# Performance work log

Hardware: AMD Instinct MI355X
Metric: run time of the kernel (lower is better)

Reference implementation:

```python
import jax, jax.numpy as jnp
import numpy as np

DICE_TH = 0.4
CLS_TH = 0.5
LN_EPS = 1e-5


def setup_inputs() -> dict:
    key = jax.random.key(0)
    P, C, NC, K = 200_000, 256, 200, 24  # points, clicks, classes, latent prototypes
    ks = jax.random.split(key, 6)
    # structured masks: each click targets one of K prototype regions so the
    # dice/cls thresholds yield a non-degenerate grouping
    point_proto = jax.random.randint(ks[0], (P,), 0, K)
    proto_vals = jax.random.uniform(ks[1], (P,))
    click_proto = jax.random.randint(ks[2], (C,), 0, K)
    base = (point_proto[:, None] == click_proto[None, :]).astype(jnp.float32)  # [P, C]
    noise = jax.random.uniform(ks[3], (P, C))
    masks_heatmap = base * (0.6 + 0.4 * proto_vals[:, None]) + 0.02 * noise
    class_emb = jax.random.normal(ks[4], (K, NC)) * 3.0
    cls_logits = class_emb[click_proto] + 0.3 * jax.random.normal(ks[5], (C, NC))
    clicks_list = jax.random.randint(ks[0], (C,), 0, NC)  # unused (random_clicks=True)
    return {"masks_heatmap": masks_heatmap, "cls_logits": cls_logits,
            "clicks_list": clicks_list}


def _associate(masks_heatmap, cls_logits):
    """Greedy dice+cls-similarity grouping (random_clicks=True path).
    Returns labels[c] = leader click index of the group containing click c."""
    M = masks_heatmap                      # [P, C]
    C = M.shape[1]
    s = M.sum(0)                           # [C]
    # dice[i, j] = 2 * m_i . m_j / (sum(m_i) + sum(m_j))  (all pairs at once)
    dice = 2.0 * (M.T @ M) / (s[:, None] + s[None, :])
    # F.layer_norm over last dim, no affine
    mu = cls_logits.mean(-1, keepdims=True)
    var = ((cls_logits - mu) ** 2).mean(-1, keepdims=True)
    p = (cls_logits - mu) / jnp.sqrt(var + LN_EPS)
    sim = p @ p.T                          # [C, C]
    cond = (dice > DICE_TH) & (sim > CLS_TH)

    def step(carry, x):
        assigned, labels = carry
        i, row = x
        # skip if i already suppressed; take unsuppressed clicks matching row i
        take = row & (~assigned) & (~assigned[i])
        return (assigned | take, jnp.where(take, i, labels)), None

    init = (jnp.zeros((C,), bool), jnp.full((C,), -1, jnp.int32))
    (assigned, labels), _ = jax.lax.scan(
        step, init, (jnp.arange(C, dtype=jnp.int32), cond))
    return labels


def _merge(labels, masks_heatmap, cls_logits):
    """reduction='max': per-group max over member clicks. Unused group slots
    (non-leader indices) are zero-filled and flagged by group_valid."""
    C = masks_heatmap.shape[1]
    seg = jnp.where(labels >= 0, labels, C)  # route unassigned to dump segment
    counts = jax.ops.segment_sum(jnp.ones((C,), jnp.float32), seg,
                                 num_segments=C + 1)[:C]
    group_valid = counts > 0
    nm = jax.ops.segment_max(masks_heatmap.T, seg, num_segments=C + 1)[:C]  # [C, P]
    nc = jax.ops.segment_max(cls_logits, seg, num_segments=C + 1)[:C]      # [C, NC]
    new_masks = jnp.where(group_valid[:, None], nm, 0.0).T  # [P, C]
    new_cls = jnp.where(group_valid[:, None], nc, 0.0)      # [C, NC]
    return new_masks, new_cls, group_valid


def reference(masks_heatmap, cls_logits, clicks_list):
    labels = _associate(masks_heatmap, cls_logits)
    new_masks, new_cls, group_valid = _merge(labels, masks_heatmap, cls_logits)
    return labels, group_valid, new_masks, new_cls
```

## Files before the change

kernel.cpp:

```cpp
#include <hip/hip_runtime.h>
#include <cstdint>
#include <cstddef>

constexpr int P  = 200000;
constexpr int C  = 256;
constexpr int NC = 200;
#define DICE_TH 0.4f
#define CLS_TH  0.5f
#define LN_EPS  1e-5f

constexpr int KC = 1600;
constexpr int NCHUNK = 125;
constexpr int NSTEP = KC / 32;

constexpr size_t WS_G       = 0;
constexpr size_t WS_S       = 262144;
constexpr size_t WS_PROW    = 263168;
constexpr size_t WS_PT      = 467968;
constexpr size_t WS_COND    = 672768;
constexpr size_t WS_MSTART  = 680960;
constexpr size_t WS_MEMBERS = 682240;
constexpr size_t WS_PART    = 1048576;
constexpr size_t PART_BYTES = (size_t)NCHUNK * 3 * 16384 * 4;

typedef float floatx4 __attribute__((ext_vector_type(4)));
typedef float floatx16 __attribute__((ext_vector_type(16)));
typedef __bf16 bf16x4 __attribute__((ext_vector_type(4)));
typedef __bf16 bf16x8 __attribute__((ext_vector_type(8)));
typedef unsigned short ushort4v __attribute__((ext_vector_type(4)));
typedef unsigned short ushort8 __attribute__((ext_vector_type(8)));

constexpr int LDA = 40;

__global__ __launch_bounds__(256, 2) void gram_mfma_kernel(
    const float* __restrict__ M, float* __restrict__ G, float* __restrict__ s,
    float* __restrict__ part) {
  __shared__ unsigned short Abf[128 * LDA];
  __shared__ unsigned short Bbf[128 * LDA];
  __shared__ float scol[128];

  const int type = blockIdx.x;
  const int i0 = (type == 2) ? 128 : 0;
  const int j0 = (type == 0) ? 0 : 128;
  const bool diag = (type != 1);
  const int tid = threadIdx.x;
  const int wv = tid >> 6, lane = tid & 63;
  const int wr = wv >> 1, wc = wv & 1;
  const int g  = tid & 31;
  const int kq = tid >> 5;
  const int chunk = blockIdx.y;
  const int k0 = chunk * KC;

  if (tid < 128) scol[tid] = 0.f;

  floatx16 acc[4];
#pragma unroll
  for (int t = 0; t < 4; ++t)
#pragma unroll
    for (int r = 0; r < 16; ++r) acc[t][r] = 0.f;
  float ss[4] = {0.f, 0.f, 0.f, 0.f};

  const int mrow = lane & 31;
  const int kgrp = (lane >> 5) * 8;
  const int xa = ((mrow >> 2) & 3) << 1;
  const int wbase = (kq ^ ((g & 3) << 1)) << 2;

  const float* baseA = M + i0 + 4 * g;
  const float* baseB = M + j0 + 4 * g;

#define LOADS(dst, base, step_)                                              \
  {                                                                          \
    const float* src_ = (base) + (size_t)(k0 + (step_) * 32 + 4 * kq) * 256; \
    dst[0] = *reinterpret_cast<const floatx4*>(src_);                        \
    dst[1] = *reinterpret_cast<const floatx4*>(src_ + 256);                  \
    dst[2] = *reinterpret_cast<const floatx4*>(src_ + 512);                  \
    dst[3] = *reinterpret_cast<const floatx4*>(src_ + 768);                  \
  }

#define STAGE(dstLds, r_)                                                    \
  {                                                                          \
    _Pragma("unroll") for (int cc = 0; cc < 4; ++cc) {                       \
      floatx4 f = {r_[0][cc], r_[1][cc], r_[2][cc], r_[3][cc]};              \
      bf16x4 b = __builtin_convertvector(f, bf16x4);                         \
      *reinterpret_cast<ushort4v*>(&dstLds[(4 * g + cc) * LDA + wbase]) =    \
          __builtin_bit_cast(ushort4v, b);                                   \
    }                                                                        \
  }

#define SSUM(r_)                                                             \
  if (diag) {                                                                \
    ss[0] += r_[0][0] + r_[1][0] + r_[2][0] + r_[3][0];                      \
    ss[1] += r_[0][1] + r_[1][1] + r_[2][1] + r_[3][1];                      \
    ss[2] += r_[0][2] + r_[1][2] + r_[2][2] + r_[3][2];                      \
    ss[3] += r_[0][3] + r_[1][3] + r_[2][3] + r_[3][3];                      \
  }

#define MFMA_STEP()                                                          \
  {                                                                          \
    const unsigned short* Bsrc = diag ? Abf : Bbf;                           \
    _Pragma("unroll") for (int sub = 0; sub < 2; ++sub) {                    \
      const int ko = sub * 16 + kgrp;                                        \
      const int koff = (((ko >> 2) ^ xa) << 2);                              \
      bf16x8 av0 = __builtin_bit_cast(                                       \
          bf16x8, *reinterpret_cast<const ushort8*>(                         \
                      &Abf[(64 * wr + mrow) * LDA + koff]));                 \
      bf16x8 av1 = __builtin_bit_cast(                                       \
          bf16x8, *reinterpret_cast<const ushort8*>(                         \
                      &Abf[(64 * wr + 32 + mrow) * LDA + koff]));            \
      bf16x8 bv0 = __builtin_bit_cast(                                       \
          bf16x8, *reinterpret_cast<const ushort8*>(                         \
                      &Bsrc[(64 * wc + mrow) * LDA + koff]));                \
      bf16x8 bv1 = __builtin_bit_cast(                                       \
          bf16x8, *reinterpret_cast<const ushort8*>(                         \
                      &Bsrc[(64 * wc + 32 + mrow) * LDA + koff]));           \
      acc[0] = __builtin_amdgcn_mfma_f32_32x32x16_bf16(av0, bv0, acc[0], 0, 0, 0); \
      acc[1] = __builtin_amdgcn_mfma_f32_32x32x16_bf16(av0, bv1, acc[1], 0, 0, 0); \
      acc[2] = __builtin_amdgcn_mfma_f32_32x32x16_bf16(av1, bv0, acc[2], 0, 0, 0); \
      acc[3] = __builtin_amdgcn_mfma_f32_32x32x16_bf16(av1, bv1, acc[3], 0, 0, 0); \
    }                                                                        \
  }

  floatx4 a0[4], a1[4], b0[4], b1[4];
  LOADS(a0, baseA, 0);
  if (!diag) LOADS(b0, baseB, 0);

  for (int sp = 0; sp < NSTEP; sp += 2) {
    SSUM(a0);
    STAGE(Abf, a0);
    if (!diag) STAGE(Bbf, b0);
    __syncthreads();
    LOADS(a1, baseA, sp + 1);
    if (!diag) LOADS(b1, baseB, sp + 1);
    MFMA_STEP();
    __syncthreads();

    SSUM(a1);
    STAGE(Abf, a1);
    if (!diag) STAGE(Bbf, b1);
    __syncthreads();
    if (sp + 2 < NSTEP) {
      LOADS(a0, baseA, sp + 2);
      if (!diag) LOADS(b0, baseB, sp + 2);
    }
    MFMA_STEP();
    __syncthreads();
  }
#undef LOADS
#undef STAGE
#undef SSUM
#undef MFMA_STEP

  if (part != nullptr) {
    float* Pp = part + ((size_t)chunk * 3 + type) * 16384;
#pragma unroll
    for (int ai = 0; ai < 2; ++ai)
#pragma unroll
      for (int bj = 0; bj < 2; ++bj)
#pragma unroll
        for (int r = 0; r < 16; ++r) {
          const int lr = 64 * wr + 32 * ai + (r & 3) + 8 * (r >> 2) + 4 * (lane >> 5);
          const int lc = 64 * wc + 32 * bj + (lane & 31);
          Pp[lr * 128 + lc] = acc[ai * 2 + bj][r];
        }
  } else {
#pragma unroll
    for (int ai = 0; ai < 2; ++ai)
#pragma unroll
      for (int bj = 0; bj < 2; ++bj)
#pragma unroll
        for (int r = 0; r < 16; ++r) {
          const int gr = i0 + 64 * wr + 32 * ai + (r & 3) + 8 * (r >> 2) + 4 * (lane >> 5);
          const int gc = j0 + 64 * wc + 32 * bj + (lane & 31);
          atomicAdd(&G[(size_t)gr * 256 + gc], acc[ai * 2 + bj][r]);
        }
  }
  if (diag) {
#pragma unroll
    for (int cc = 0; cc < 4; ++cc) atomicAdd(&scol[4 * g + cc], ss[cc]);
    __syncthreads();
    if (tid < 128) atomicAdd(&s[i0 + tid], scol[tid]);
  }
}

__global__ __launch_bounds__(128) void reduce_g_kernel(
    const float* __restrict__ part, float* __restrict__ G) {
  const int slot = blockIdx.x >> 7;
  const int lr = blockIdx.x & 127;
  const int lc = threadIdx.x;
  const float* src = part + (size_t)slot * 16384 + (size_t)lr * 128 + lc;
  float s0 = 0.f, s1 = 0.f, s2 = 0.f, s3 = 0.f, s4 = 0.f;
  int ch = 0;
  for (; ch + 5 <= NCHUNK; ch += 5) {
    s0 += src[(size_t)(ch + 0) * 49152];
    s1 += src[(size_t)(ch + 1) * 49152];
    s2 += src[(size_t)(ch + 2) * 49152];
    s3 += src[(size_t)(ch + 3) * 49152];
    s4 += src[(size_t)(ch + 4) * 49152];
  }
  for (; ch < NCHUNK; ++ch) s0 += src[(size_t)ch * 49152];
  const int i0 = (slot == 2) ? 128 : 0;
  const int j0 = (slot == 0) ? 0 : 128;
  G[(size_t)(i0 + lr) * 256 + (j0 + lc)] = ((s0 + s1) + (s2 + s3)) + s4;
}

__global__ __launch_bounds__(64) void ln_kernel(const float* __restrict__ cls,
                                                float* __restrict__ p_row,
                                                float* __restrict__ pT) {
  const int c = blockIdx.x;
  const int t = threadIdx.x;
  const float* x = cls + (size_t)c * NC;
  float v0 = x[t];
  float v1 = x[t + 64];
  float v2 = (t < 72) ? x[t + 128] : 0.f;

  float sum = v0 + v1 + v2;
#pragma unroll
  for (int o = 32; o > 0; o >>= 1) sum += __shfl_xor(sum, o);
  const float mu = sum / (float)NC;

  float d0 = v0 - mu, d1 = v1 - mu, d2 = (t < 72) ? (v2 - mu) : 0.f;
  float sq = d0 * d0 + d1 * d1 + d2 * d2;
#pragma unroll
  for (int o = 32; o > 0; o >>= 1) sq += __shfl_xor(sq, o);
  const float var = sq / (float)NC;
  const float inv = 1.0f / sqrtf(var + LN_EPS);

  float p0 = d0 * inv, p1 = d1 * inv, p2 = d2 * inv;
  p_row[(size_t)c * NC + t] = p0;
  p_row[(size_t)c * NC + t + 64] = p1;
  pT[(size_t)t * C + c] = p0;
  pT[(size_t)(t + 64) * C + c] = p1;
  if (t < 72) {
    p_row[(size_t)c * NC + t + 128] = p2;
    pT[(size_t)(t + 128) * C + c] = p2;
  }
}

__global__ __launch_bounds__(256) void cond_kernel(
    const float* __restrict__ G, const float* __restrict__ s,
    const float* __restrict__ p_row, const float* __restrict__ pT,
    unsigned long long* __restrict__ condW) {
  __shared__ float pi[NC];
  const int i = blockIdx.x;
  const int j = threadIdx.x;
  if (j < NC) pi[j] = p_row[(size_t)i * NC + j];
  __syncthreads();

  const float si = s[i];
  const float sj = s[j];
  const float g = (i >= 128 && j < 128) ? G[(size_t)j * C + i]
                                        : G[(size_t)i * C + j];
  const float dice = 2.f * g / (si + sj);

  float acc = 0.f;
#pragma unroll 8
  for (int k = 0; k < NC; ++k) acc = fmaf(pi[k], pT[(size_t)k * C + j], acc);

  const bool cnd = (dice > DICE_TH) && (acc > CLS_TH);
  unsigned long long m = __ballot(cnd);
  if ((j & 63) == 0) condW[i * 4 + (j >> 6)] = m;
}

__global__ __launch_bounds__(64) void scan_kernel(
    const unsigned long long* __restrict__ condW,
    float* __restrict__ out_labels, float* __restrict__ out_valid,
    int* __restrict__ mstart, int* __restrict__ members) {
  __shared__ unsigned long long cS[C * 4];
  __shared__ int cnt[C];
  __shared__ int ms[C + 1];
  const int t = threadIdx.x;

  for (int idx = t; idx < C * 4; idx += 64) cS[idx] = condW[idx];
  for (int idx = t; idx < C; idx += 64) cnt[idx] = 0;
  __syncthreads();

  unsigned long long asg[4] = {0ull, 0ull, 0ull, 0ull};
  int lab[4] = {-1, -1, -1, -1};

#pragma unroll
  for (int w = 0; w < 4; ++w) {
    for (int b = 0; b < 64; ++b) {
      const int i = w * 64 + b;
      if (!((asg[w] >> b) & 1ull)) {
#pragma unroll
        for (int w2 = 0; w2 < 4; ++w2) {
          unsigned long long tk = cS[i * 4 + w2] & ~asg[w2];
          asg[w2] |= tk;
          if ((tk >> t) & 1ull) lab[w2] = i;
        }
      }
    }
  }

#pragma unroll
  for (int w = 0; w < 4; ++w)
    if (lab[w] >= 0) atomicAdd(&cnt[lab[w]], 1);
  __syncthreads();

  if (t == 0) {
    ms[0] = 0;
    for (int c2 = 0; c2 < C; ++c2) ms[c2 + 1] = ms[c2] + cnt[c2];
  }
  __syncthreads();
  for (int idx = t; idx < C; idx += 64) cnt[idx] = ms[idx];
  __syncthreads();
#pragma unroll
  for (int w = 0; w < 4; ++w) {
    if (lab[w] >= 0) {
      int pos = atomicAdd(&cnt[lab[w]], 1);
      members[pos] = w * 64 + t;
    }
  }
#pragma unroll
  for (int w = 0; w < 4; ++w) {
    const int col = w * 64 + t;
    out_labels[col] = (float)lab[w];
    out_valid[col] = (ms[col + 1] > ms[col]) ? 1.0f : 0.0f;
  }
  for (int idx = t; idx < C + 1; idx += 64) mstart[idx] = ms[idx];
}

constexpr int MROWS = 8;

__global__ __launch_bounds__(256) void merge_masks_kernel(
    const float* __restrict__ M, const int* __restrict__ mstart,
    const int* __restrict__ members, float* __restrict__ out_masks) {
  __shared__ float rows[MROWS * 256];
  __shared__ int msS[C + 1];
  __shared__ int memS[C];
  const int tid = threadIdx.x;
  const size_t p0 = (size_t)blockIdx.x * MROWS;

  msS[tid] = mstart[tid];
  if (tid == 0) msS[C] = mstart[C];
  memS[tid] = members[tid];

  const float4* src = reinterpret_cast<const float4*>(M + p0 * 256);
#pragma unroll
  for (int it = 0; it < MROWS / 4; ++it)
    reinterpret_cast<float4*>(rows)[it * 256 + tid] = src[it * 256 + tid];
  __syncthreads();

  const int st = msS[tid], en = msS[tid + 1];
  float mx[MROWS];
  if (en > st) {
    const int m0 = memS[st];
#pragma unroll
    for (int r = 0; r < MROWS; ++r) mx[r] = rows[r * 256 + m0];
    for (int k = st + 1; k < en; ++k) {
      const int mm = memS[k];
#pragma unroll
      for (int r = 0; r < MROWS; ++r) mx[r] = fmaxf(mx[r], rows[r * 256 + mm]);
    }
  } else {
#pragma unroll
    for (int r = 0; r < MROWS; ++r) mx[r] = 0.f;
  }
  __syncthreads();
#pragma unroll
  for (int r = 0; r < MROWS; ++r) rows[r * 256 + tid] = mx[r];
  __syncthreads();

  const int r2 = tid >> 6;
  const int cg = (tid & 63) << 2;
#pragma unroll
  for (int pass = 0; pass < MROWS / 4; ++pass) {
    const int rr = pass * 4 + r2;
    floatx4 v = *reinterpret_cast<const floatx4*>(&rows[rr * 256 + cg]);
    __builtin_nontemporal_store(
        v, reinterpret_cast<floatx4*>(&out_masks[(p0 + rr) * 256 + cg]));
  }
}

__global__ __launch_bounds__(256) void merge_cls_kernel(
    const float* __restrict__ cls, const int* __restrict__ mstart,
    const int* __restrict__ members, float* __restrict__ out_cls) {
  __shared__ int se[2];
  const int c = blockIdx.x;
  const int t = threadIdx.x;
  if (t < 2) se[t] = mstart[c + t];
  __syncthreads();
  const int st = se[0], en = se[1];
  if (t < NC) {
    float mx = 0.f;
    if (en > st) {
      mx = cls[(size_t)members[st] * NC + t];
      for (int k = st + 1; k < en; ++k)
        mx = fmaxf(mx, cls[(size_t)members[k] * NC + t]);
    }
    out_cls[(size_t)c * NC + t] = mx;
  }
}

extern "C" void kernel_launch(void* const* d_in, const int* in_sizes, int n_in,
                              void* d_out, int out_size, void* d_ws,
                              size_t ws_size, hipStream_t stream) {
  const float* M = (const float*)d_in[0];
  const float* cls = (const float*)d_in[1];

  float* out = (float*)d_out;
  char* ws = (char*)d_ws;
  float* G = (float*)(ws + WS_G);
  float* s = (float*)(ws + WS_S);
  float* p_row = (float*)(ws + WS_PROW);
  float* pT = (float*)(ws + WS_PT);
  unsigned long long* condW = (unsigned long long*)(ws + WS_COND);
  int* mstart = (int*)(ws + WS_MSTART);
  int* members = (int*)(ws + WS_MEMBERS);

  float* out_labels = out;
  float* out_valid = out + 256;
  float* out_masks = out + 512;
  float* out_cls = out + 512 + (size_t)P * 256;

  const bool bigws = ws_size >= WS_PART + PART_BYTES;
  float* part = bigws ? (float*)(ws + WS_PART) : nullptr;

  if (bigws) {
    hipMemsetAsync(ws + WS_S, 0, 1024, stream);
  } else {
    hipMemsetAsync(ws, 0, WS_S + 1024, stream);
  }

  gram_mfma_kernel<<<dim3(3, NCHUNK), 256, 0, stream>>>(M, G, s, part);
  if (bigws) reduce_g_kernel<<<384, 128, 0, stream>>>(part, G);
  ln_kernel<<<C, 64, 0, stream>>>(cls, p_row, pT);
  cond_kernel<<<C, 256, 0, stream>>>(G, s, p_row, pT, condW);
  scan_kernel<<<1, 64, 0, stream>>>(condW, out_labels, out_valid, mstart,
                                    members);
  merge_masks_kernel<<<P / MROWS, 256, 0, stream>>>(M, mstart, members,
                                                    out_masks);
  merge_cls_kernel<<<C, 256, 0, stream>>>(cls, mstart, members, out_cls);
}
```

Before: 419.4 us.

## Remap gram blocks for XCD locality and fuse partial reduction into cond kernel

The gram kernel now uses a 1D grid of 384 blocks. Blocks are remapped so that all three tile types of a chunk, and contiguous chunks, land on the same XCD (bid & 7), which improves L2 sharing of the M rows. The separate reduce_g launch is removed, and cond_kernel now sums the 125 per-chunk partials itself for each (i,j) element. This saves one launch and one round trip for G, but the partial reduction now runs in 256 blocks, with strided loads per thread in place of a dedicated kernel.

```diff
diff --git a/kernel.cpp b/kernel.cpp
--- a/kernel.cpp
+++ b/kernel.cpp
@@ -35,11 +35,21 @@
 __global__ __launch_bounds__(256, 2) void gram_mfma_kernel(
     const float* __restrict__ M, float* __restrict__ G, float* __restrict__ s,
     float* __restrict__ part) {
+  const int bid = blockIdx.x;
+  const int xcd = bid & 7;
+  const int slot = bid >> 3;
+  constexpr int q = NCHUNK / 8, r = NCHUNK % 8;
+  const int nch = (xcd < r) ? q + 1 : q;
+  const int ci = slot / 3;
+  if (ci >= nch) return;
+  const int cbase = (xcd < r) ? xcd * (q + 1) : r * (q + 1) + (xcd - r) * q;
+  const int chunk = cbase + ci;
+  const int type = slot - 3 * ci;
+
   __shared__ unsigned short Abf[128 * LDA];
   __shared__ unsigned short Bbf[128 * LDA];
   __shared__ float scol[128];
 
-  const int type = blockIdx.x;
   const int i0 = (type == 2) ? 128 : 0;
   const int j0 = (type == 0) ? 0 : 128;
   const bool diag = (type != 1);
@@ -48,7 +58,6 @@
   const int wr = wv >> 1, wc = wv & 1;
   const int g  = tid & 31;
   const int kq = tid >> 5;
-  const int chunk = blockIdx.y;
   const int k0 = chunk * KC;
 
   if (tid < 128) scol[tid] = 0.f;
@@ -57,7 +66,7 @@
 #pragma unroll
   for (int t = 0; t < 4; ++t)
 #pragma unroll
-    for (int r = 0; r < 16; ++r) acc[t][r] = 0.f;
+    for (int r2 = 0; r2 < 16; ++r2) acc[t][r2] = 0.f;
   float ss[4] = {0.f, 0.f, 0.f, 0.f};
 
   const int mrow = lane & 31;
@@ -157,10 +166,10 @@
 #pragma unroll
       for (int bj = 0; bj < 2; ++bj)
 #pragma unroll
-        for (int r = 0; r < 16; ++r) {
-          const int lr = 64 * wr + 32 * ai + (r & 3) + 8 * (r >> 2) + 4 * (lane >> 5);
+        for (int r2 = 0; r2 < 16; ++r2) {
+          const int lr = 64 * wr + 32 * ai + (r2 & 3) + 8 * (r2 >> 2) + 4 * (lane >> 5);
           const int lc = 64 * wc + 32 * bj + (lane & 31);
-          Pp[lr * 128 + lc] = acc[ai * 2 + bj][r];
+          Pp[lr * 128 + lc] = acc[ai * 2 + bj][r2];
         }
   } else {
 #pragma unroll
@@ -168,10 +177,10 @@
 #pragma unroll
       for (int bj = 0; bj < 2; ++bj)
 #pragma unroll
-        for (int r = 0; r < 16; ++r) {
-          const int gr = i0 + 64 * wr + 32 * ai + (r & 3) + 8 * (r >> 2) + 4 * (lane >> 5);
+        for (int r2 = 0; r2 < 16; ++r2) {
+          const int gr = i0 + 64 * wr + 32 * ai + (r2 & 3) + 8 * (r2 >> 2) + 4 * (lane >> 5);
           const int gc = j0 + 64 * wc + 32 * bj + (lane & 31);
-          atomicAdd(&G[(size_t)gr * 256 + gc], acc[ai * 2 + bj][r]);
+          atomicAdd(&G[(size_t)gr * 256 + gc], acc[ai * 2 + bj][r2]);
         }
   }
   if (diag) {
@@ -180,27 +189,6 @@
     __syncthreads();
     if (tid < 128) atomicAdd(&s[i0 + tid], scol[tid]);
   }
-}
-
-__global__ __launch_bounds__(128) void reduce_g_kernel(
-    const float* __restrict__ part, float* __restrict__ G) {
-  const int slot = blockIdx.x >> 7;
-  const int lr = blockIdx.x & 127;
-  const int lc = threadIdx.x;
-  const float* src = part + (size_t)slot * 16384 + (size_t)lr * 128 + lc;
-  float s0 = 0.f, s1 = 0.f, s2 = 0.f, s3 = 0.f, s4 = 0.f;
-  int ch = 0;
-  for (; ch + 5 <= NCHUNK; ch += 5) {
-    s0 += src[(size_t)(ch + 0) * 49152];
-    s1 += src[(size_t)(ch + 1) * 49152];
-    s2 += src[(size_t)(ch + 2) * 49152];
-    s3 += src[(size_t)(ch + 3) * 49152];
-    s4 += src[(size_t)(ch + 4) * 49152];
-  }
-  for (; ch < NCHUNK; ++ch) s0 += src[(size_t)ch * 49152];
-  const int i0 = (slot == 2) ? 128 : 0;
-  const int j0 = (slot == 0) ? 0 : 128;
-  G[(size_t)(i0 + lr) * 256 + (j0 + lc)] = ((s0 + s1) + (s2 + s3)) + s4;
 }
 
 __global__ __launch_bounds__(64) void ln_kernel(const float* __restrict__ cls,
@@ -237,20 +225,43 @@
 }
 
 __global__ __launch_bounds__(256) void cond_kernel(
-    const float* __restrict__ G, const float* __restrict__ s,
-    const float* __restrict__ p_row, const float* __restrict__ pT,
-    unsigned long long* __restrict__ condW) {
+    const float* __restrict__ G, const float* __restrict__ part,
+    const float* __restrict__ s, const float* __restrict__ p_row,
+    const float* __restrict__ pT, unsigned long long* __restrict__ condW) {
   __shared__ float pi[NC];
   const int i = blockIdx.x;
   const int j = threadIdx.x;
   if (j < NC) pi[j] = p_row[(size_t)i * NC + j];
   __syncthreads();
 
+  float gsum;
+  if (part != nullptr) {
+    int type, lr, lc;
+    if (i < 128) {
+      if (j < 128) { type = 0; lr = i; lc = j; }
+      else         { type = 1; lr = i; lc = j - 128; }
+    } else {
+      if (j >= 128) { type = 2; lr = i - 128; lc = j - 128; }
+      else          { type = 1; lr = j; lc = i - 128; }
+    }
+    const float* src = part + (size_t)type * 16384 + (size_t)lr * 128 + lc;
+    float s0 = 0.f, s1 = 0.f, s2 = 0.f, s3 = 0.f, s4 = 0.f;
+#pragma unroll 1
+    for (int ch = 0; ch + 5 <= NCHUNK; ch += 5) {
+      s0 += src[(size_t)(ch + 0) * 49152];
+      s1 += src[(size_t)(ch + 1) * 49152];
+      s2 += src[(size_t)(ch + 2) * 49152];
+      s3 += src[(size_t)(ch + 3) * 49152];
+      s4 += src[(size_t)(ch + 4) * 49152];
+    }
+    gsum = ((s0 + s1) + (s2 + s3)) + s4;
+  } else {
+    gsum = (i >= 128 && j < 128) ? G[(size_t)j * C + i] : G[(size_t)i * C + j];
+  }
+
   const float si = s[i];
   const float sj = s[j];
-  const float g = (i >= 128 && j < 128) ? G[(size_t)j * C + i]
-                                        : G[(size_t)i * C + j];
-  const float dice = 2.f * g / (si + sj);
+  const float dice = 2.f * gsum / (si + sj);
 
   float acc = 0.f;
 #pragma unroll 8
@@ -422,10 +433,9 @@
     hipMemsetAsync(ws, 0, WS_S + 1024, stream);
   }
 
-  gram_mfma_kernel<<<dim3(3, NCHUNK), 256, 0, stream>>>(M, G, s, part);
-  if (bigws) reduce_g_kernel<<<384, 128, 0, stream>>>(part, G);
+  gram_mfma_kernel<<<384, 256, 0, stream>>>(M, G, s, part);
   ln_kernel<<<C, 64, 0, stream>>>(cls, p_row, pT);
-  cond_kernel<<<C, 256, 0, stream>>>(G, s, p_row, pT, condW);
+  cond_kernel<<<C, 256, 0, stream>>>(G, part, s, p_row, pT, condW);
   scan_kernel<<<1, 64, 0, stream>>>(condW, out_labels, out_valid, mstart,
                                     members);
   merge_masks_kernel<<<P / MROWS, 256, 0, stream>>>(M, mstart, members,
```

After: 435.3 us. 1.04x slower.
